# Optimization experiments

Hardware: AMD Instinct MI355X
Metric: run time of the kernel (lower is better)

Reference implementation:

```python
import jax, jax.numpy as jnp
import numpy as np
import math

# init config (matches init_kwargs); sigma/alpha are squared in __init__
SIGMA2 = 8.0 ** 2
ALPHA2 = 8.0 ** 2
C_SIZE = 512
STRIDE = 8
MINX = 1e-06
M = 100                      # ratio=100 > 1 -> M = int(ratio), capped at 100
K = C_SIZE // STRIDE         # 64 grid cells per axis
G = K * K                    # 4096 density-field cells
B, N = 8, 512                # images, annotated points per image
TWO_PI = 2.0 * math.pi


def setup_inputs():
    key = jax.random.key(0)
    k1, _ = jax.random.split(key)
    points = jax.random.uniform(k1, (B, N, 2), dtype=jnp.float32) * C_SIZE
    st_sizes = jnp.full((B,), float(C_SIZE), dtype=jnp.float32)
    return {"points": points, "st_sizes": st_sizes}


def _per_image(pts, cood):
    # pts: [N,2]; cood: [K]
    x = pts[:, 0]
    y = pts[:, 1]
    dx = x[:, None] - cood[None, :]                 # [N,K]
    dy = y[:, None] - cood[None, :]                 # [N,K]
    # dis_all = y_dis[:, :, None] + x_dis[:, None, :] flattened: g = iy*K + ix
    dis = (dy[:, :, None] ** 2 + dx[:, None, :] ** 2).reshape(pts.shape[0], G)  # [N,G]
    s1 = ALPHA2 + SIGMA2
    s2 = ALPHA2 + SIGMA2 / 2.0
    m = jnp.exp(-0.5 / s1 * dis) / (TWO_PI * s1)    # [N,G]
    tv = jnp.exp(-0.5 / s2 * dis) / (TWO_PI * s2)
    v = (tv / (TWO_PI * 2.0 * SIGMA2)).sum(0) - (m ** 2).sum(0)   # [G] (sel_v == v, no bg)
    # top-M cells by sel_v, then sort indices ascending (ratio>1 branch -> static M)
    inds = jnp.argsort(-v)
    Minds = jnp.sort(inds[:M])                      # [M]
    v = jnp.maximum(v, MINX)                        # add=False -> clamp
    # xf[n, iy*K+ix] = x_n - cood[ix]; yf[n, iy*K+ix] = y_n - cood[iy]
    iy = Minds // K
    ix = Minds % K
    xfM = dx[:, ix]                                 # [N,M]
    yfM = dy[:, iy]                                 # [N,M]
    df = (xfM[:, None, :] - xfM[:, :, None]) ** 2 + (yfM[:, None, :] - yfM[:, :, None]) ** 2
    af = (0.5 * (xfM[:, None, :] + xfM[:, :, None])) ** 2 + (0.5 * (yfM[:, None, :] + yfM[:, :, None])) ** 2
    g1 = jnp.exp(-0.5 / (2.0 * SIGMA2) * df) / (TWO_PI * 2.0 * SIGMA2)          # [N,M,M]
    tmpv2 = (g1 * (jnp.exp(-0.5 / s2 * af) / (TWO_PI * s2))).sum(0) + g1.sum(0)  # [M,M]
    disM = dis[:, Minds]                            # [N,M]
    tmpm2 = jnp.exp(-0.5 / s1 * disM) / (TWO_PI * s1)
    A = tmpv2 - tmpm2.T @ tmpm2                     # [M,M]
    eye = jnp.eye(M, dtype=bool)
    A = jnp.where(eye, 1e-10, A)                    # diag overwritten to 1e-10
    vM = v[Minds] + 1e-10
    tmpA = vM[:, None] * jnp.linalg.inv(A) * vM[None, :] + jnp.diag(vM)
    Bm = jnp.linalg.inv(tmpA)
    return m, v, A, Bm, Minds


def reference(points, st_sizes):
    # st_sizes only matters for use_background=True; kept for signature fidelity
    cood = jnp.arange(0, C_SIZE, STRIDE, dtype=jnp.float32) + STRIDE / 2.0
    m, v, A, Bm, Minds = jax.vmap(lambda p: _per_image(p, cood))(points)
    return m, v, A, Bm, Minds
```

## Files before the change

kernel.cpp:

```cpp
#include <hip/hip_runtime.h>
#include <math.h>

#ifndef M_PI
#define M_PI 3.14159265358979323846
#endif

#define BB 8
#define NN 512
#define KK 64
#define GG 4096
#define MM 100

#define SZ_VD    (BB*GG*8u*4u)
#define OFF_VD   0u
#define SZ_VM    (BB*MM*4u)
#define OFF_VM   (OFF_VD + SZ_VD)
#define SZ_AD    (BB*MM*MM*4u*2u)
#define OFF_AD   (OFF_VM + SZ_VM)

#define OUT_M  0
#define OUT_V  (BB*NN*GG)
#define OUT_A  (OUT_V + BB*GG)
#define OUT_B  (OUT_A + BB*MM*MM)
#define OUT_MI (OUT_B + BB*MM*MM)

#define MU_PER 8
#define MU_VP 4096
#define MU_AS 2048
#define MU_IV 10240

__device__ __forceinline__ void m_units(const float* __restrict__ pts,
                                        float* __restrict__ out, int u0, int cnt) {
  const float CM = (float)(1.0/(2.0*M_PI*128.0));
  for (int k = 0; k < cnt; ++k) {
    int u = u0 + k;
    int t = u*256 + (int)threadIdx.x;
    int e = t << 2;
    int img = e >> 21;
    int rem = e & ((1 << 21) - 1);
    int n = rem >> 12;
    int g = rem & 4095;
    int iy = g >> 6, ix = g & 63;
    float x = pts[(img*NN + n)*2 + 0];
    float y = pts[(img*NN + n)*2 + 1];
    float dy = y - (8.0f*iy + 4.0f);
    float ey = __expf(dy*dy*(-0.5f/128.0f));
    float4 r;
    float dx0 = x - (8.0f*ix + 4.0f);
    float dx1 = x - (8.0f*(ix+1) + 4.0f);
    float dx2 = x - (8.0f*(ix+2) + 4.0f);
    float dx3 = x - (8.0f*(ix+3) + 4.0f);
    r.x = ey*__expf(dx0*dx0*(-0.5f/128.0f))*CM;
    r.y = ey*__expf(dx1*dx1*(-0.5f/128.0f))*CM;
    r.z = ey*__expf(dx2*dx2*(-0.5f/128.0f))*CM;
    r.w = ey*__expf(dx3*dx3*(-0.5f/128.0f))*CM;
    *reinterpret_cast<float4*>(&out[OUT_M + e]) = r;
  }
}

__device__ __forceinline__ void m_units512(const float* __restrict__ pts,
                                           float* __restrict__ out, int u0, int cnt) {
  const float CM = (float)(1.0/(2.0*M_PI*128.0));
  for (int k = 0; k < cnt/2; ++k) {
    int t = u0*256 + k*512 + (int)threadIdx.x;
    int e = t << 2;
    int img = e >> 21;
    int rem = e & ((1 << 21) - 1);
    int n = rem >> 12;
    int g = rem & 4095;
    int iy = g >> 6, ix = g & 63;
    float x = pts[(img*NN + n)*2 + 0];
    float y = pts[(img*NN + n)*2 + 1];
    float dy = y - (8.0f*iy + 4.0f);
    float ey = __expf(dy*dy*(-0.5f/128.0f));
    float4 r;
    float dx0 = x - (8.0f*ix + 4.0f);
    float dx1 = x - (8.0f*(ix+1) + 4.0f);
    float dx2 = x - (8.0f*(ix+2) + 4.0f);
    float dx3 = x - (8.0f*(ix+3) + 4.0f);
    r.x = ey*__expf(dx0*dx0*(-0.5f/128.0f))*CM;
    r.y = ey*__expf(dx1*dx1*(-0.5f/128.0f))*CM;
    r.z = ey*__expf(dx2*dx2*(-0.5f/128.0f))*CM;
    r.w = ey*__expf(dx3*dx3*(-0.5f/128.0f))*CM;
    *reinterpret_cast<float4*>(&out[OUT_M + e]) = r;
  }
}

__device__ __forceinline__ float flt_readlane(float v, int l) {
  return __int_as_float(__builtin_amdgcn_readlane(__float_as_int(v), l));
}

__global__ __launch_bounds__(256) void k_vpart(const float* __restrict__ pts,
                                               double* __restrict__ vd,
                                               float* __restrict__ out) {
  __shared__ double sEy2[16][66], sEy3[16][66], sEx2[16][66], sEx3[16][66];
  __shared__ float px[128], py[128];
  int bid = blockIdx.x;
  if (bid >= BB*64) { m_units(pts, out, (bid - BB*64)*MU_PER, MU_PER); return; }
  int quarter = bid & 3;
  int rem = bid >> 2;
  int tile = rem & 15;
  int img = rem >> 4;
  int iy0 = (tile >> 2) << 4;
  int ix0 = (tile & 3) << 4;
  int tx = threadIdx.x & 15, ty = threadIdx.x >> 4;
  int n = threadIdx.x & 63;
  int tbl = threadIdx.x >> 6;
  if (threadIdx.x < 128) {
    px[threadIdx.x] = pts[(img*NN + quarter*128 + threadIdx.x)*2 + 0];
    py[threadIdx.x] = pts[(img*NN + quarter*128 + threadIdx.x)*2 + 1];
  }
  const double alpha = (tbl & 1) ? (1.0/128.0) : (0.5/96.0);
  const double Q = exp(-128.0*alpha);
  const int base = (tbl >= 2) ? ix0 : iy0;
  double* dst = (tbl == 0) ? &sEy2[0][0] : (tbl == 1) ? &sEy3[0][0]
              : (tbl == 2) ? &sEx2[0][0] : &sEx3[0][0];
  double aV = 0.0, aM = 0.0;
  for (int kc = 0; kc < 2; ++kc) {
    int nbl = kc << 6;
    __syncthreads();
    {
      int nn = nbl + n;
      double coord = (tbl >= 2) ? (double)px[nn] : (double)py[nn];
      double d0 = coord - (8.0*base + 4.0);
      double E = exp(-alpha*d0*d0);
      double R = exp(alpha*(16.0*d0 - 64.0));
      #pragma unroll
      for (int row = 0; row < 16; ++row) {
        dst[row*66 + n] = E;
        E *= R; R *= Q;
      }
    }
    __syncthreads();
    #pragma unroll 8
    for (int n2 = 0; n2 < 64; n2 += 2) {
      double2 y2 = *reinterpret_cast<const double2*>(&sEy2[ty][n2]);
      double2 x2 = *reinterpret_cast<const double2*>(&sEx2[tx][n2]);
      double2 y3 = *reinterpret_cast<const double2*>(&sEy3[ty][n2]);
      double2 x3 = *reinterpret_cast<const double2*>(&sEx3[tx][n2]);
      aV += y2.x*x2.x; aV += y2.y*x2.y;
      aM += y3.x*x3.x; aM += y3.y*x3.y;
    }
  }
  const double CTV = 1.0/((2.0*M_PI*96.0)*(2.0*M_PI*128.0));
  const double CM2 = 1.0/((2.0*M_PI*128.0)*(2.0*M_PI*128.0));
  vd[quarter*(BB*GG) + img*GG + (iy0 + ty)*KK + ix0 + tx] = CTV*aV - CM2*aM;
}

union AselU {
  struct {
    unsigned int ku[GG];
    unsigned int hist[32][257];
    unsigned int wq[4];
    unsigned int sPref, sMask;
    unsigned int sRem, sPickB, sPickRem, sCGt, sCEq;
    int tie[128];
  } se;
  struct {
    float sxi[16][130], syi[16][130], sti[16][130];
    float sxj[16][130], syj[16][130], stj[16][130];
    float px[NN], py[NN];
    float cxi[16], cyi[16], cxj[16], cyj[16];
  } ka;
};

__device__ __forceinline__ void wave_sort128(int* a) {
  int L = (int)(threadIdx.x & 63);
  int e0 = a[2*L], e1 = a[2*L + 1];
  for (int kk = 2; kk <= 128; kk <<= 1) {
    for (int jj = kk >> 1; jj >= 2; jj >>= 1) {
      int pl = jj >> 1;
      int o0 = __shfl_xor(e0, pl);
      int o1 = __shfl_xor(e1, pl);
      bool upper = (L & pl) != 0;
      bool up = ((2*L) & kk) == 0;
      if (up != upper) { e0 = min(e0, o0); e1 = min(e1, o1); }
      else             { e0 = max(e0, o0); e1 = max(e1, o1); }
    }
    bool up = ((2*L) & kk) == 0;
    int lo = min(e0, e1), hi = max(e0, e1);
    e0 = up ? lo : hi; e1 = up ? hi : lo;
  }
  a[2*L] = e0; a[2*L + 1] = e1;
}

__global__ __launch_bounds__(256) void k_Asel(const float* __restrict__ pts,
                                              const double* __restrict__ vd,
                                              float* __restrict__ out,
                                              float* __restrict__ ad,
                                              float* __restrict__ vm) {
  __shared__ AselU u;
  __shared__ int selFinal[128];
  int bid = blockIdx.x;
  if (bid >= BB*56) { m_units(pts, out, MU_VP + (bid - BB*56)*MU_PER, MU_PER); return; }
  int img = bid / 56;
  int rem56 = bid - img*56;
  int tile = rem56 >> 1;
  int half = rem56 & 1;
  bool emit = (tile == 0) && (half == 0);
  int tid = threadIdx.x;
  int wv = tid >> 6;
  int lane = tid & 63;
  int hc = tid >> 3;

  for (int t = 0; t < 16; ++t) {
    int g = t*256 + tid;
    float v = (float)(((vd[img*GG + g] + vd[BB*GG + img*GG + g])
                     + vd[2*BB*GG + img*GG + g]) + vd[3*BB*GG + img*GG + g]);
    if (emit) out[OUT_V + img*GG + g] = fmaxf(v, 1e-6f);
    int w = __float_as_int(v);
    u.se.ku[g] = (w < 0) ? ~(unsigned)w : ((unsigned)w | 0x80000000u);
  }
  if (tid == 0) {
    u.se.sRem = 100; u.se.sPref = 0u; u.se.sMask = 0u;
    u.se.sCGt = 0; u.se.sCEq = 0;
  }
  for (int shift = 24; shift >= 0; shift -= 8) {
    for (int s = tid; s < 32*257; s += 256) (&u.se.hist[0][0])[s] = 0;
    __syncthreads();
    unsigned mask = u.se.sMask, pref = u.se.sPref;
    for (int t = 0; t < 16; ++t) {
      unsigned k = u.se.ku[t*256 + tid];
      if ((k & mask) == pref)
        atomicAdd(&u.se.hist[hc][(k >> shift) & 255u], 1u);
    }
    __syncthreads();
    unsigned tot = 0;
    #pragma unroll
    for (int c = 0; c < 32; ++c) tot += u.se.hist[c][tid];
    unsigned val = tot;
    #pragma unroll
    for (int off = 1; off < 64; off <<= 1) {
      unsigned o = (unsigned)__shfl_down((int)val, off);
      if (lane + off < 64) val += o;
    }
    if (lane == 0) u.se.wq[wv] = val;
    __syncthreads();
    unsigned suf = val;
    for (int w2 = wv + 1; w2 < 4; ++w2) suf += u.se.wq[w2];
    unsigned rem = u.se.sRem;
    unsigned sgt = suf - tot;
    if (suf >= rem && sgt < rem) { u.se.sPickB = (unsigned)tid; u.se.sPickRem = rem - sgt; }
    __syncthreads();
    if (tid == 0) {
      u.se.sPref |= u.se.sPickB << shift;
      u.se.sMask |= 255u << shift;
      u.se.sRem   = u.se.sPickRem;
    }
    __syncthreads();
  }
  unsigned T = u.se.sPref;
  for (int t = 0; t < 16; ++t) {
    int g = t*256 + tid;
    unsigned k = u.se.ku[g];
    if (k > T) {
      unsigned p = atomicAdd(&u.se.sCGt, 1u);
      selFinal[p] = g;
    } else if (k == T) {
      unsigned p = atomicAdd(&u.se.sCEq, 1u);
      if (p < 128) u.se.tie[p] = g;
    }
  }
  __syncthreads();
  unsigned cgt = u.se.sCGt, ceq = u.se.sCEq, r = u.se.sRem;
  if (tid < 128 && tid >= (int)((ceq < 128u) ? ceq : 128u)) u.se.tie[tid] = 0x7fffffff;
  __syncthreads();
  if (tid < 64) wave_sort128(u.se.tie);
  __syncthreads();
  if (tid < (int)r) selFinal[cgt + tid] = u.se.tie[tid];
  if (tid >= MM && tid < 128) selFinal[tid] = 0x7fffffff;
  __syncthreads();
  if (tid < 64) wave_sort128(selFinal);
  __syncthreads();
  if (emit && tid < MM) {
    int mi = selFinal[tid];
    out[OUT_MI + img*MM + tid] = (float)mi;
    float vsel = (float)(((vd[img*GG + mi] + vd[BB*GG + img*GG + mi])
                        + vd[2*BB*GG + img*GG + mi]) + vd[3*BB*GG + img*GG + mi]);
    vm[img*MM + tid] = fmaxf(vsel, 1e-6f) + 1e-10f;
  }
  __syncthreads();

  int it = 0, trem = tile;
  while (trem >= 7 - it) { trem -= 7 - it; ++it; }
  int jt = it + trem;
  int i0 = it*16, j0 = jt*16;
  int tj = tid & 15, ti = tid >> 4;
  int i = i0 + ti, j = j0 + tj;
  const float CM = (float)(1.0/(2.0*M_PI*128.0));
  const float C1 = (float)(1.0/(2.0*M_PI*128.0));
  const float C2 = (float)(1.0/(2.0*M_PI*96.0));
  for (int s = tid; s < NN; s += 256) {
    u.ka.px[s] = pts[(img*NN + s)*2 + 0];
    u.ka.py[s] = pts[(img*NN + s)*2 + 1];
  }
  if (tid < 16) {
    int gi = i0 + tid; if (gi > 99) gi = 99;
    int mi = selFinal[gi];
    u.ka.cxi[tid] = 8.0f*(mi & 63) + 4.0f;
    u.ka.cyi[tid] = 8.0f*(mi >> 6) + 4.0f;
  } else if (tid < 32) {
    int rr = tid - 16;
    int gj = j0 + rr; if (gj > 99) gj = 99;
    int mj = selFinal[gj];
    u.ka.cxj[rr] = 8.0f*(mj & 63) + 4.0f;
    u.ka.cyj[rr] = 8.0f*(mj >> 6) + 4.0f;
  }
  float aV = 0.0f, aM = 0.0f;
  for (int nc = half*256; nc < half*256 + 256; nc += 128) {
    __syncthreads();
    for (int s = tid; s < 16*128; s += 256) {
      int row = s >> 7, n = s & 127;
      float x = u.ka.px[nc + n], y = u.ka.py[nc + n];
      float fxi = x - u.ka.cxi[row], fyi = y - u.ka.cyi[row];
      u.ka.sxi[row][n] = fxi; u.ka.syi[row][n] = fyi;
      u.ka.sti[row][n] = __expf((fxi*fxi + fyi*fyi)*(-0.5f/128.0f))*CM;
      float fxj = x - u.ka.cxj[row], fyj = y - u.ka.cyj[row];
      u.ka.sxj[row][n] = fxj; u.ka.syj[row][n] = fyj;
      u.ka.stj[row][n] = __expf((fxj*fxj + fyj*fyj)*(-0.5f/128.0f))*CM;
    }
    __syncthreads();
    #pragma unroll 4
    for (int n = 0; n < 128; ++n) {
      float xi = u.ka.sxi[ti][n], yi = u.ka.syi[ti][n], tii = u.ka.sti[ti][n];
      float xj = u.ka.sxj[tj][n], yj = u.ka.syj[tj][n], tjj = u.ka.stj[tj][n];
      float ddx = xj - xi, ddy = yj - yi;
      float df = ddx*ddx + ddy*ddy;
      float sx = 0.5f*(xi + xj), sy = 0.5f*(yi + yj);
      float af = sx*sx + sy*sy;
      float g1 = __expf(df*(-0.5f/128.0f))*C1;
      float h  = __expf(af*(-0.5f/96.0f))*C2;
      aV += g1 + g1*h;
      aM += tii*tjj;
    }
  }
  if (i < 100 && j < 100) {
    float val = (i == j) ? 1e-10f : (float)((double)aV - (double)aM);
    ad[((half*BB + img)*MM + i)*MM + j] = val;
    if (it != jt) {
      ad[((half*BB + img)*MM + j)*MM + i] = val;
    }
  }
}

#define PRS 130
__global__ __launch_bounds__(512)
void k_inv_m(const float* __restrict__ ad,
             const float* __restrict__ vm,
             const float* __restrict__ pts,
             float* __restrict__ out) {
  __shared__ float S[128*17];
  __shared__ float Pr[16*PRS];
  __shared__ float svm[112];
  if (blockIdx.x >= BB) {
    m_units512(pts, out, MU_VP + MU_AS + ((int)blockIdx.x - BB)*MU_PER, MU_PER);
    return;
  }
  int img = blockIdx.x;
  int tx = threadIdx.x & 31, ty = threadIdx.x >> 5;
  float C[7][4];
  if (threadIdx.x < 100) svm[threadIdx.x] = vm[img*MM + threadIdx.x];
  #pragma unroll
  for (int a = 0; a < 7; ++a) {
    int r = ty + 16*a;
    #pragma unroll
    for (int b = 0; b < 4; ++b) {
      int col = tx + 32*b;
      float v2 = 0.0f;
      if (r < 100 && col < 100) {
        if (r == col) {
          v2 = 1e-10f + vm[img*MM + r];
          out[OUT_A + (img*MM + r)*MM + col] = 1e-10f;
        } else {
          float s = ad[(img*MM + r)*MM + col] + ad[((BB + img)*MM + r)*MM + col];
          v2 = s;
          out[OUT_A + (img*MM + r)*MM + col] = s;
        }
      }
      C[a][b] = v2;
    }
  }
  for (int p = 0; p < 7; ++p) {
    int k0 = p*16;
    int nbp = (p == 6) ? 4 : 16;
    {
      int bp = p >> 1;
      bool mine = ((tx >> 4) == (p & 1));
      int cq = tx & 15;
      #pragma unroll
      for (int a = 0; a < 7; ++a) {
        int r = ty + 16*a;
        if (mine) {
          float val = 0.0f;
          #pragma unroll
          for (int b = 0; b < 4; ++b) if (b == bp) val = C[a][b];
          S[r*17 + cq] = (r < 100 && cq < nbp) ? val : 0.0f;
        }
      }
    }
    {
      float pv[4];
      #pragma unroll
      for (int b = 0; b < 4; ++b) pv[b] = 0.0f;
      #pragma unroll
      for (int a = 0; a < 7; ++a) {
        #pragma unroll
        for (int b = 0; b < 4; ++b) if (a == p) pv[b] = C[a][b];
      }
      #pragma unroll
      for (int b = 0; b < 4; ++b) Pr[ty*PRS + tx + 32*b] = pv[b];
    }
    __syncthreads();
    if (threadIdx.x < 64) {
      int lane = threadIdx.x;
      float P0[16], P1[16];
      #pragma unroll
      for (int c = 0; c < 16; ++c) {
        P0[c] = S[lane*17 + c];
        P1[c] = (lane + 64 < 112) ? S[(lane + 64)*17 + c] : 0.0f;
      }
      #pragma unroll
      for (int kk = 0; kk < 16; ++kk) {
        if (kk < nbp) {
          int kg = k0 + kk;
          int r1 = lane + 64;
          bool khigh = kg >= 64; int kl = kg & 63;
          float pivinv = 1.0f / flt_readlane(khigh ? P1[kk] : P0[kk], kl);
          float pr[16];
          #pragma unroll
          for (int c = 0; c < 16; ++c) {
            float pv = flt_readlane(khigh ? P1[c] : P0[c], kl);
            pr[c] = (c == kk) ? pivinv : pv*pivinv;
          }
          {
            float f = P0[kk];
            if (lane == kg) {
              #pragma unroll
              for (int c = 0; c < 16; ++c) P0[c] = pr[c];
            } else {
              #pragma unroll
              for (int c = 0; c < 16; ++c) P0[c] = ((c == kk) ? 0.0f : P0[c]) - f*pr[c];
            }
          }
          {
            float f = P1[kk];
            if (r1 == kg) {
              #pragma unroll
              for (int c = 0; c < 16; ++c) P1[c] = pr[c];
            } else {
              #pragma unroll
              for (int c = 0; c < 16; ++c) P1[c] = ((c == kk) ? 0.0f : P1[c]) - f*pr[c];
            }
          }
        }
      }
      #pragma unroll
      for (int c = 0; c < 16; ++c) {
        S[lane*17 + c] = P0[c];
        if (lane + 64 < 112) S[(lane + 64)*17 + c] = P1[c];
      }
    }
    __syncthreads();
    #pragma unroll
    for (int a = 0; a < 7; ++a) {
      int r = ty + 16*a;
      bool prow_ = (r >= k0) && (r < k0 + 16);
      #pragma unroll
      for (int b = 0; b < 4; ++b) {
        int col = tx + 32*b;
        if (r >= 100 || (col >> 4) == p || prow_) C[a][b] = 0.0f;
      }
    }
    #pragma unroll 4
    for (int t = 0; t < 16; ++t) {
      bool tok = (t < nbp);
      float bt[4], sa[7];
      #pragma unroll
      for (int b = 0; b < 4; ++b) bt[b] = tok ? Pr[t*PRS + tx + 32*b] : 0.0f;
      #pragma unroll
      for (int a = 0; a < 7; ++a) sa[a] = S[(ty + 16*a)*17 + t];
      #pragma unroll
      for (int a = 0; a < 7; ++a)
        #pragma unroll
        for (int b = 0; b < 4; ++b) C[a][b] += sa[a]*bt[b];
    }
    #pragma unroll
    for (int a = 0; a < 7; ++a) {
      int r = ty + 16*a;
      #pragma unroll
      for (int b = 0; b < 4; ++b) {
        int col = tx + 32*b;
        if ((col >> 4) == p) C[a][b] = S[r*17 + (col & 15)];
      }
    }
    __syncthreads();
  }
  #pragma unroll
  for (int a = 0; a < 7; ++a) {
    int r = ty + 16*a; if (r >= 100) continue;
    float dinv = 1.0f / svm[r];
    #pragma unroll
    for (int b = 0; b < 4; ++b) {
      int col = tx + 32*b; if (col >= 100) continue;
      float val = ((col == r) ? dinv : 0.0f) - C[a][b];
      out[OUT_B + (img*MM + r)*MM + col] = val;
    }
  }
}

extern "C" void kernel_launch(void* const* d_in, const int* in_sizes, int n_in,
                              void* d_out, int out_size, void* d_ws, size_t ws_size,
                              hipStream_t stream) {
  const float* pts = (const float*)d_in[0];
  float* out = (float*)d_out;
  char* ws = (char*)d_ws;
  double* vd  = (double*)(ws + OFF_VD);
  float* vmd = (float*)(ws + OFF_VM);
  float* ad  = (float*)(ws + OFF_AD);

  hipLaunchKernelGGL(k_vpart, dim3(BB*64 + MU_VP/MU_PER), dim3(256), 0, stream, pts, vd, out);
  hipLaunchKernelGGL(k_Asel, dim3(BB*56 + MU_AS/MU_PER), dim3(256), 0, stream, pts, vd, out, ad, vmd);
  hipLaunchKernelGGL(k_inv_m, dim3(BB + MU_IV/MU_PER), dim3(512), 0, stream, ad, vmd, pts, out);
}
```

Before: 190.4 us.

## Split top-M selection from A-matrix kernel to avoid redundant per-tile selection

Before this change, each of the 56 tile blocks per image redid the full radix top-100 selection over 4096 cells. That selection now runs once per image in a new k_select kernel, which writes the chosen indices to workspace. A separate k_A kernel reads those indices and computes the A tiles. The m-filler work units are spread across the now four launches. The cost is one extra kernel launch and a serialization point, where k_select runs on only 8 real blocks plus filler work.

```diff
diff --git a/kernel.cpp b/kernel.cpp
--- a/kernel.cpp
+++ b/kernel.cpp
@@ -17,6 +17,7 @@
 #define OFF_VM   (OFF_VD + SZ_VD)
 #define SZ_AD    (BB*MM*MM*4u*2u)
 #define OFF_AD   (OFF_VM + SZ_VM)
+#define OFF_MIND (OFF_AD + SZ_AD)
 
 #define OUT_M  0
 #define OUT_V  (BB*NN*GG)
@@ -26,8 +27,9 @@
 
 #define MU_PER 8
 #define MU_VP 4096
-#define MU_AS 2048
-#define MU_IV 10240
+#define MU_SE 1024
+#define MU_KA 2048
+#define MU_IV 9216
 
 __device__ __forceinline__ void m_units(const float* __restrict__ pts,
                                         float* __restrict__ out, int u0, int cnt) {
@@ -147,23 +149,6 @@
   vd[quarter*(BB*GG) + img*GG + (iy0 + ty)*KK + ix0 + tx] = CTV*aV - CM2*aM;
 }
 
-union AselU {
-  struct {
-    unsigned int ku[GG];
-    unsigned int hist[32][257];
-    unsigned int wq[4];
-    unsigned int sPref, sMask;
-    unsigned int sRem, sPickB, sPickRem, sCGt, sCEq;
-    int tie[128];
-  } se;
-  struct {
-    float sxi[16][130], syi[16][130], sti[16][130];
-    float sxj[16][130], syj[16][130], stj[16][130];
-    float px[NN], py[NN];
-    float cxi[16], cyi[16], cxj[16], cyj[16];
-  } ka;
-};
-
 __device__ __forceinline__ void wave_sort128(int* a) {
   int L = (int)(threadIdx.x & 63);
   int e0 = a[2*L], e1 = a[2*L + 1];
@@ -184,20 +169,21 @@
   a[2*L] = e0; a[2*L + 1] = e1;
 }
 
-__global__ __launch_bounds__(256) void k_Asel(const float* __restrict__ pts,
-                                              const double* __restrict__ vd,
-                                              float* __restrict__ out,
-                                              float* __restrict__ ad,
-                                              float* __restrict__ vm) {
-  __shared__ AselU u;
+__global__ __launch_bounds__(256) void k_select(const double* __restrict__ vd,
+                                               float* __restrict__ out,
+                                               int* __restrict__ minds,
+                                               float* __restrict__ vm,
+                                               const float* __restrict__ pts) {
+  __shared__ unsigned int ku[GG];
+  __shared__ unsigned int hist[32][257];
+  __shared__ unsigned int wq[4];
+  __shared__ unsigned int sPref, sMask;
+  __shared__ unsigned int sRem, sPickB, sPickRem, sCGt, sCEq;
+  __shared__ int tie[128];
   __shared__ int selFinal[128];
   int bid = blockIdx.x;
-  if (bid >= BB*56) { m_units(pts, out, MU_VP + (bid - BB*56)*MU_PER, MU_PER); return; }
-  int img = bid / 56;
-  int rem56 = bid - img*56;
-  int tile = rem56 >> 1;
-  int half = rem56 & 1;
-  bool emit = (tile == 0) && (half == 0);
+  if (bid >= BB) { m_units(pts, out, MU_VP + (bid - BB)*MU_PER, MU_PER); return; }
+  int img = bid;
   int tid = threadIdx.x;
   int wv = tid >> 6;
   int lane = tid & 63;
@@ -207,80 +193,96 @@
     int g = t*256 + tid;
     float v = (float)(((vd[img*GG + g] + vd[BB*GG + img*GG + g])
                      + vd[2*BB*GG + img*GG + g]) + vd[3*BB*GG + img*GG + g]);
-    if (emit) out[OUT_V + img*GG + g] = fmaxf(v, 1e-6f);
+    out[OUT_V + img*GG + g] = fmaxf(v, 1e-6f);
     int w = __float_as_int(v);
-    u.se.ku[g] = (w < 0) ? ~(unsigned)w : ((unsigned)w | 0x80000000u);
+    ku[g] = (w < 0) ? ~(unsigned)w : ((unsigned)w | 0x80000000u);
   }
   if (tid == 0) {
-    u.se.sRem = 100; u.se.sPref = 0u; u.se.sMask = 0u;
-    u.se.sCGt = 0; u.se.sCEq = 0;
+    sRem = 100; sPref = 0u; sMask = 0u;
+    sCGt = 0; sCEq = 0;
   }
   for (int shift = 24; shift >= 0; shift -= 8) {
-    for (int s = tid; s < 32*257; s += 256) (&u.se.hist[0][0])[s] = 0;
-    __syncthreads();
-    unsigned mask = u.se.sMask, pref = u.se.sPref;
+    for (int s = tid; s < 32*257; s += 256) (&hist[0][0])[s] = 0;
+    __syncthreads();
+    unsigned mask = sMask, pref = sPref;
     for (int t = 0; t < 16; ++t) {
-      unsigned k = u.se.ku[t*256 + tid];
+      unsigned k = ku[t*256 + tid];
       if ((k & mask) == pref)
-        atomicAdd(&u.se.hist[hc][(k >> shift) & 255u], 1u);
+        atomicAdd(&hist[hc][(k >> shift) & 255u], 1u);
     }
     __syncthreads();
     unsigned tot = 0;
     #pragma unroll
-    for (int c = 0; c < 32; ++c) tot += u.se.hist[c][tid];
+    for (int c = 0; c < 32; ++c) tot += hist[c][tid];
     unsigned val = tot;
     #pragma unroll
     for (int off = 1; off < 64; off <<= 1) {
       unsigned o = (unsigned)__shfl_down((int)val, off);
       if (lane + off < 64) val += o;
     }
-    if (lane == 0) u.se.wq[wv] = val;
+    if (lane == 0) wq[wv] = val;
     __syncthreads();
     unsigned suf = val;
-    for (int w2 = wv + 1; w2 < 4; ++w2) suf += u.se.wq[w2];
-    unsigned rem = u.se.sRem;
+    for (int w2 = wv + 1; w2 < 4; ++w2) suf += wq[w2];
+    unsigned rem = sRem;
     unsigned sgt = suf - tot;
-    if (suf >= rem && sgt < rem) { u.se.sPickB = (unsigned)tid; u.se.sPickRem = rem - sgt; }
+    if (suf >= rem && sgt < rem) { sPickB = (unsigned)tid; sPickRem = rem - sgt; }
     __syncthreads();
     if (tid == 0) {
-      u.se.sPref |= u.se.sPickB << shift;
-      u.se.sMask |= 255u << shift;
-      u.se.sRem   = u.se.sPickRem;
-    }
-    __syncthreads();
-  }
-  unsigned T = u.se.sPref;
+      sPref |= sPickB << shift;
+      sMask |= 255u << shift;
+      sRem   = sPickRem;
+    }
+    __syncthreads();
+  }
+  unsigned T = sPref;
   for (int t = 0; t < 16; ++t) {
     int g = t*256 + tid;
-    unsigned k = u.se.ku[g];
+    unsigned k = ku[g];
     if (k > T) {
-      unsigned p = atomicAdd(&u.se.sCGt, 1u);
+      unsigned p = atomicAdd(&sCGt, 1u);
       selFinal[p] = g;
     } else if (k == T) {
-      unsigned p = atomicAdd(&u.se.sCEq, 1u);
-      if (p < 128) u.se.tie[p] = g;
+      unsigned p = atomicAdd(&sCEq, 1u);
+      if (p < 128) tie[p] = g;
     }
   }
   __syncthreads();
-  unsigned cgt = u.se.sCGt, ceq = u.se.sCEq, r = u.se.sRem;
-  if (tid < 128 && tid >= (int)((ceq < 128u) ? ceq : 128u)) u.se.tie[tid] = 0x7fffffff;
+  unsigned cgt = sCGt, ceq = sCEq, r = sRem;
+  if (tid < 128 && tid >= (int)((ceq < 128u) ? ceq : 128u)) tie[tid] = 0x7fffffff;
   __syncthreads();
-  if (tid < 64) wave_sort128(u.se.tie);
+  if (tid < 64) wave_sort128(tie);
   __syncthreads();
-  if (tid < (int)r) selFinal[cgt + tid] = u.se.tie[tid];
+  if (tid < (int)r) selFinal[cgt + tid] = tie[tid];
   if (tid >= MM && tid < 128) selFinal[tid] = 0x7fffffff;
   __syncthreads();
   if (tid < 64) wave_sort128(selFinal);
   __syncthreads();
-  if (emit && tid < MM) {
+  if (tid < MM) {
     int mi = selFinal[tid];
+    minds[img*MM + tid] = mi;
     out[OUT_MI + img*MM + tid] = (float)mi;
     float vsel = (float)(((vd[img*GG + mi] + vd[BB*GG + img*GG + mi])
                         + vd[2*BB*GG + img*GG + mi]) + vd[3*BB*GG + img*GG + mi]);
     vm[img*MM + tid] = fmaxf(vsel, 1e-6f) + 1e-10f;
   }
-  __syncthreads();
-
+}
+
+__global__ __launch_bounds__(256) void k_A(const float* __restrict__ pts,
+                                           const int* __restrict__ minds,
+                                           float* __restrict__ out,
+                                           float* __restrict__ ad) {
+  __shared__ float sxi[16][130], syi[16][130], sti[16][130];
+  __shared__ float sxj[16][130], syj[16][130], stj[16][130];
+  __shared__ float px[256], py[256];
+  __shared__ float cxi[16], cyi[16], cxj[16], cyj[16];
+  int bid = blockIdx.x;
+  if (bid >= BB*56) { m_units(pts, out, MU_VP + MU_SE + (bid - BB*56)*MU_PER, MU_PER); return; }
+  int img = bid / 56;
+  int rem56 = bid - img*56;
+  int tile = rem56 >> 1;
+  int half = rem56 & 1;
+  int tid = threadIdx.x;
   int it = 0, trem = tile;
   while (trem >= 7 - it) { trem -= 7 - it; ++it; }
   int jt = it + trem;
@@ -290,40 +292,40 @@
   const float CM = (float)(1.0/(2.0*M_PI*128.0));
   const float C1 = (float)(1.0/(2.0*M_PI*128.0));
   const float C2 = (float)(1.0/(2.0*M_PI*96.0));
-  for (int s = tid; s < NN; s += 256) {
-    u.ka.px[s] = pts[(img*NN + s)*2 + 0];
-    u.ka.py[s] = pts[(img*NN + s)*2 + 1];
+  if (tid < 256) {
+    px[tid] = pts[(img*NN + half*256 + tid)*2 + 0];
+    py[tid] = pts[(img*NN + half*256 + tid)*2 + 1];
   }
   if (tid < 16) {
     int gi = i0 + tid; if (gi > 99) gi = 99;
-    int mi = selFinal[gi];
-    u.ka.cxi[tid] = 8.0f*(mi & 63) + 4.0f;
-    u.ka.cyi[tid] = 8.0f*(mi >> 6) + 4.0f;
+    int mi = minds[img*MM + gi];
+    cxi[tid] = 8.0f*(mi & 63) + 4.0f;
+    cyi[tid] = 8.0f*(mi >> 6) + 4.0f;
   } else if (tid < 32) {
     int rr = tid - 16;
     int gj = j0 + rr; if (gj > 99) gj = 99;
-    int mj = selFinal[gj];
-    u.ka.cxj[rr] = 8.0f*(mj & 63) + 4.0f;
-    u.ka.cyj[rr] = 8.0f*(mj >> 6) + 4.0f;
+    int mj = minds[img*MM + gj];
+    cxj[rr] = 8.0f*(mj & 63) + 4.0f;
+    cyj[rr] = 8.0f*(mj >> 6) + 4.0f;
   }
   float aV = 0.0f, aM = 0.0f;
-  for (int nc = half*256; nc < half*256 + 256; nc += 128) {
+  for (int c2 = 0; c2 < 256; c2 += 128) {
     __syncthreads();
     for (int s = tid; s < 16*128; s += 256) {
       int row = s >> 7, n = s & 127;
-      float x = u.ka.px[nc + n], y = u.ka.py[nc + n];
-      float fxi = x - u.ka.cxi[row], fyi = y - u.ka.cyi[row];
-      u.ka.sxi[row][n] = fxi; u.ka.syi[row][n] = fyi;
-      u.ka.sti[row][n] = __expf((fxi*fxi + fyi*fyi)*(-0.5f/128.0f))*CM;
-      float fxj = x - u.ka.cxj[row], fyj = y - u.ka.cyj[row];
-      u.ka.sxj[row][n] = fxj; u.ka.syj[row][n] = fyj;
-      u.ka.stj[row][n] = __expf((fxj*fxj + fyj*fyj)*(-0.5f/128.0f))*CM;
+      float x = px[c2 + n], y = py[c2 + n];
+      float fxi = x - cxi[row], fyi = y - cyi[row];
+      sxi[row][n] = fxi; syi[row][n] = fyi;
+      sti[row][n] = __expf((fxi*fxi + fyi*fyi)*(-0.5f/128.0f))*CM;
+      float fxj = x - cxj[row], fyj = y - cyj[row];
+      sxj[row][n] = fxj; syj[row][n] = fyj;
+      stj[row][n] = __expf((fxj*fxj + fyj*fyj)*(-0.5f/128.0f))*CM;
     }
     __syncthreads();
     #pragma unroll 4
     for (int n = 0; n < 128; ++n) {
-      float xi = u.ka.sxi[ti][n], yi = u.ka.syi[ti][n], tii = u.ka.sti[ti][n];
-      float xj = u.ka.sxj[tj][n], yj = u.ka.syj[tj][n], tjj = u.ka.stj[tj][n];
+      float xi = sxi[ti][n], yi = syi[ti][n], tii = sti[ti][n];
+      float xj = sxj[tj][n], yj = syj[tj][n], tjj = stj[tj][n];
       float ddx = xj - xi, ddy = yj - yi;
       float df = ddx*ddx + ddy*ddy;
       float sx = 0.5f*(xi + xj), sy = 0.5f*(yi + yj);
@@ -353,7 +355,7 @@
   __shared__ float Pr[16*PRS];
   __shared__ float svm[112];
   if (blockIdx.x >= BB) {
-    m_units512(pts, out, MU_VP + MU_AS + ((int)blockIdx.x - BB)*MU_PER, MU_PER);
+    m_units512(pts, out, MU_VP + MU_SE + MU_KA + ((int)blockIdx.x - BB)*MU_PER, MU_PER);
     return;
   }
   int img = blockIdx.x;
@@ -517,8 +519,10 @@
   double* vd  = (double*)(ws + OFF_VD);
   float* vmd = (float*)(ws + OFF_VM);
   float* ad  = (float*)(ws + OFF_AD);
+  int* minds = (int*)(ws + OFF_MIND);
 
   hipLaunchKernelGGL(k_vpart, dim3(BB*64 + MU_VP/MU_PER), dim3(256), 0, stream, pts, vd, out);
-  hipLaunchKernelGGL(k_Asel, dim3(BB*56 + MU_AS/MU_PER), dim3(256), 0, stream, pts, vd, out, ad, vmd);
+  hipLaunchKernelGGL(k_select, dim3(BB + MU_SE/MU_PER), dim3(256), 0, stream, vd, out, minds, vmd, pts);
+  hipLaunchKernelGGL(k_A, dim3(BB*56 + MU_KA/MU_PER), dim3(256), 0, stream, pts, minds, out, ad);
   hipLaunchKernelGGL(k_inv_m, dim3(BB + MU_IV/MU_PER), dim3(512), 0, stream, ad, vmd, pts, out);
 }
```

After: 188.5 us. Within noise of the previous version (-1.0%).
